# Optimization experiments

Hardware: AMD Instinct MI355X
Metric: run time of the kernel (lower is better)

Reference implementation:

```python
import jax, jax.numpy as jnp
import numpy as np

D_IN = 1024
D_OUT = 1024
NUM_HEADS = 16
HEAD_DIM = D_OUT // NUM_HEADS
SEQ = 2048
BATCH = 2


def setup_inputs() -> dict:
    key = jax.random.key(0)
    ks = jax.random.split(key, 6)
    s = 1.0 / np.sqrt(D_IN)
    x = jax.random.normal(ks[0], (BATCH, SEQ, D_IN), dtype=jnp.float32)
    Wq = jax.random.uniform(ks[1], (D_IN, D_OUT), jnp.float32, -s, s)
    Wk = jax.random.uniform(ks[2], (D_IN, D_OUT), jnp.float32, -s, s)
    Wv = jax.random.uniform(ks[3], (D_IN, D_OUT), jnp.float32, -s, s)
    Wo = jax.random.uniform(ks[4], (D_OUT, D_OUT), jnp.float32, -s, s)
    bo = jax.random.uniform(ks[5], (D_OUT,), jnp.float32, -s, s)
    return {"x": x, "Wq": Wq, "Wk": Wk, "Wv": Wv, "Wo": Wo, "bo": bo}


def reference(x, Wq, Wk, Wv, Wo, bo):
    b, n, _ = x.shape
    # projections, split into heads: (b, h, n, hd)
    def split_heads(t):
        return t.reshape(b, n, NUM_HEADS, HEAD_DIM).transpose(0, 2, 1, 3)
    q = split_heads(x @ Wq)
    k = split_heads(x @ Wk)
    v = split_heads(x @ Wv)
    scores = jnp.einsum("bhqd,bhkd->bhqk", q, k)
    causal = jnp.triu(jnp.ones((n, n), dtype=bool), k=1)
    scores = jnp.where(causal, -jnp.inf, scores)
    attn = jax.nn.softmax(scores / np.sqrt(HEAD_DIM), axis=-1)
    # dropout prob is 0.0 -> identity
    ctx = jnp.einsum("bhqk,bhkd->bhqd", attn, v)
    ctx = ctx.transpose(0, 2, 1, 3).reshape(b, n, D_OUT)
    return ctx @ Wo + bo
```

## Files before the change

kernel.cpp:

```cpp
#include <hip/hip_runtime.h>
#include <hip/hip_bf16.h>
#include <stdint.h>

#define D_IN   1024
#define D_OUT  1024
#define NHEAD  16
#define HDIM   64
#define SEQ    2048
#define BATCH  2
#define M_TOT  (BATCH*SEQ)

typedef __attribute__((ext_vector_type(8)))  short bfx8;
typedef __attribute__((ext_vector_type(4)))  short bfx4;
typedef __attribute__((ext_vector_type(4)))  float fx4;
typedef __attribute__((ext_vector_type(16))) float fx16;
typedef unsigned short u16;
typedef unsigned int   u32;

__device__ __forceinline__ u16 f2bf(float f) {
    u32 u = __builtin_bit_cast(u32, f);
    u32 r = (u + 0x7FFFu + ((u >> 16) & 1u)) >> 16;
    return (u16)r;
}

__device__ __forceinline__ u32 cvtpk(float lo, float hi) {
    u32 r;
    asm("v_cvt_pk_bf16_f32 %0, %1, %2" : "=v"(r) : "v"(lo), "v"(hi));
    return r;
}

__device__ __forceinline__ void gload16(const u16* g, u16* l) {
    __builtin_amdgcn_global_load_lds(
        (const __attribute__((address_space(1))) void*)g,
        (__attribute__((address_space(3))) void*)l, 16, 0, 0);
}

__global__ void k_conv_x(const float* __restrict__ x, u16* __restrict__ xb) {
    int i = blockIdx.x * 256 + threadIdx.x;
    const float4* s = reinterpret_cast<const float4*>(x);
    float4 a = s[2*i], b = s[2*i+1];
    uint4 o;
    o.x = (u32)f2bf(a.x) | ((u32)f2bf(a.y) << 16);
    o.y = (u32)f2bf(a.z) | ((u32)f2bf(a.w) << 16);
    o.z = (u32)f2bf(b.x) | ((u32)f2bf(b.y) << 16);
    o.w = (u32)f2bf(b.z) | ((u32)f2bf(b.w) << 16);
    reinterpret_cast<uint4*>(xb)[i] = o;
}

__global__ void k_conv_wt(const float* __restrict__ Wq, const float* __restrict__ Wk,
                          const float* __restrict__ Wv, const float* __restrict__ Wo,
                          u16* __restrict__ wt) {
    __shared__ float tile[32][33];
    int wsel = blockIdx.z;
    const float* W = (wsel == 0) ? Wq : (wsel == 1) ? Wk : (wsel == 2) ? Wv : Wo;
    const float scale = (wsel == 0) ? 0.125f : 1.0f;
    u16* dst = wt + (size_t)wsel * D_IN * D_OUT;
    int r0 = blockIdx.y * 32, c0 = blockIdx.x * 32;
    int tx = threadIdx.x & 31, ty = threadIdx.x >> 5;
    #pragma unroll
    for (int k = 0; k < 4; k++) {
        int i = ty + k * 8;
        tile[i][tx] = W[(size_t)(r0 + i) * D_OUT + c0 + tx];
    }
    __syncthreads();
    #pragma unroll
    for (int k = 0; k < 4; k++) {
        int i = ty + k * 8;
        dst[(size_t)(c0 + i) * D_IN + r0 + tx] = f2bf(tile[tx][i] * scale);
    }
}

template<int MODE>
__global__ __launch_bounds__(256) void k_gemm128(const u16* __restrict__ A,
                                                 const u16* __restrict__ Bt,
                                                 const float* __restrict__ bias,
                                                 u16* __restrict__ outb,
                                                 float* __restrict__ outf) {
    __shared__ u16 aL[128][32];
    __shared__ u16 bL[128][32];
    const int K = 1024;
    const int nb = blockIdx.x * 128, mb = blockIdx.y * 128;
    const int t = threadIdx.x, lane = t & 63, w = t >> 6;
    const int wr = w >> 1, wc = w & 1;
    const int li = lane & 15, lg = lane >> 4;
    const int srow = lane >> 2, schunk = (lane & 3) * 8;

    fx4 acc[4][4];
    #pragma unroll
    for (int i = 0; i < 4; i++)
        #pragma unroll
        for (int j = 0; j < 4; j++) acc[i][j] = fx4{0.f, 0.f, 0.f, 0.f};

    const u16* aBase = A  + (size_t)(mb + w * 32 + srow) * K + schunk;
    const u16* bBase = Bt + (size_t)(nb + w * 32 + srow) * K + schunk;

    for (int kb = 0; kb < K; kb += 32) {
        #pragma unroll
        for (int c = 0; c < 2; c++) {
            gload16(aBase + (size_t)c * 16 * K + kb, &aL[w * 32 + c * 16][0]);
            gload16(bBase + (size_t)c * 16 * K + kb, &bL[w * 32 + c * 16][0]);
        }
        __syncthreads();
        bfx8 af[4], bf[4];
        #pragma unroll
        for (int mi = 0; mi < 4; mi++)
            af[mi] = *reinterpret_cast<const bfx8*>(&aL[wr * 64 + mi * 16 + li][lg * 8]);
        #pragma unroll
        for (int ni = 0; ni < 4; ni++)
            bf[ni] = *reinterpret_cast<const bfx8*>(&bL[wc * 64 + ni * 16 + li][lg * 8]);
        #pragma unroll
        for (int mi = 0; mi < 4; mi++)
            #pragma unroll
            for (int ni = 0; ni < 4; ni++)
                acc[mi][ni] = __builtin_amdgcn_mfma_f32_16x16x32_bf16(af[mi], bf[ni], acc[mi][ni], 0, 0, 0);
        __syncthreads();
    }

    #pragma unroll
    for (int mi = 0; mi < 4; mi++) {
        #pragma unroll
        for (int ni = 0; ni < 4; ni++) {
            const int n = nb + wc * 64 + ni * 16 + li;
            const int m0 = mb + wr * 64 + mi * 16 + lg * 4;
            if (MODE == 0) {
                const int proj = n >> 10, h = (n >> 6) & 15, d = n & 63;
                const int b = m0 >> 11, s0 = m0 & 2047;
                if (proj == 2) {
                    u16* op = outb + (size_t)2 * M_TOT * D_OUT +
                              ((size_t)(b * NHEAD + h) * HDIM + d) * SEQ + s0;
                    bfx4 pk = {(short)f2bf(acc[mi][ni][0]), (short)f2bf(acc[mi][ni][1]),
                               (short)f2bf(acc[mi][ni][2]), (short)f2bf(acc[mi][ni][3])};
                    *reinterpret_cast<bfx4*>(op) = pk;
                } else {
                    u16* op = outb + (size_t)proj * M_TOT * D_OUT;
                    #pragma unroll
                    for (int r = 0; r < 4; r++)
                        op[((size_t)(b * NHEAD + h) * SEQ + s0 + r) * HDIM + d] =
                            f2bf(acc[mi][ni][r]);
                }
            } else {
                const float bv = bias[n];
                #pragma unroll
                for (int r = 0; r < 4; r++)
                    outf[(size_t)(m0 + r) * D_OUT + n] = acc[mi][ni][r] + bv;
            }
        }
    }
}

__global__ __launch_bounds__(128, 2) void k_attn(const u16* __restrict__ Q,
                                                 const u16* __restrict__ Kp,
                                                 const u16* __restrict__ Vt,
                                                 u16* __restrict__ ctx) {
    __shared__ u16 kbuf[2][64][64];
    __shared__ u16 vbuf[2][64][64];

    const int g    = blockIdx.x;
    const int pid  = g & 255, half = g >> 8;
    const int bh   = pid & 31, jb = pid >> 5;
    const int qi   = (half == 0) ? jb : (half == 1) ? (31 - jb)
                   : (half == 2) ? (8 + jb) : (23 - jb);
    const int ntk  = qi + 1;

    const size_t base = (size_t)bh * SEQ * HDIM;
    const int t = threadIdx.x, lane = t & 63, w = t >> 6;
    const int l31 = lane & 31, hi = lane >> 5;
    const int srow = lane >> 3;
    const int ts = (lane & 7) ^ srow;
    const int bq = bh >> 4, hh = bh & 15;
    const int swz = (l31 & 7) * 8;
    const int qwb = qi * 64 + w * 32;
    const int qg  = qwb + l31;

    auto stage = [&](int bi, int kvb) {
        #pragma unroll
        for (int i = 0; i < 4; i++) {
            const int rb = w * 32 + i * 8;
            const int rr = rb + srow;
            gload16(Kp + base + (size_t)(kvb + rr) * HDIM + ts * 8, &kbuf[bi][rb][0]);
            gload16(Vt + base + (size_t)rr * SEQ + kvb + ts * 8,    &vbuf[bi][rb][0]);
        }
    };

    bfx8 qf[4];
    #pragma unroll
    for (int dc = 0; dc < 4; dc++)
        qf[dc] = *reinterpret_cast<const bfx8*>(
            &Q[base + (size_t)qg * HDIM + dc * 16 + hi * 8]);
    fx16 cacc[2];
    #pragma unroll
    for (int dt = 0; dt < 2; dt++)
        #pragma unroll
        for (int r = 0; r < 16; r++) cacc[dt][r] = 0.f;
    float lsum = 0.f;

    stage(0, 0);
    __syncthreads();

    for (int ti = 0; ti < ntk; ti++) {
        if (ti + 1 < ntk) stage((ti + 1) & 1, (ti + 1) * 64);
        const int bi = ti & 1, kvb = ti * 64;
        fx16 sc[2];
        #pragma unroll
        for (int s = 0; s < 2; s++) {
            #pragma unroll
            for (int r = 0; r < 16; r++) sc[s][r] = 0.f;
            #pragma unroll
            for (int dc = 0; dc < 4; dc++) {
                bfx8 kf = *reinterpret_cast<const bfx8*>(
                    &kbuf[bi][s * 32 + l31][(dc * 16 + hi * 8) ^ swz]);
                sc[s] = __builtin_amdgcn_mfma_f32_32x32x16_bf16(kf, qf[dc], sc[s], 0, 0, 0);
            }
        }
        if (kvb + 63 > qwb) {
            #pragma unroll
            for (int s = 0; s < 2; s++)
                #pragma unroll
                for (int r = 0; r < 16; r++) {
                    int kvg = kvb + s * 32 + (r & 3) + 8 * (r >> 2) + 4 * hi;
                    if (kvg > qg) sc[s][r] = -1e30f;
                }
        }
        float ps = 0.f;
        #pragma unroll
        for (int s = 0; s < 2; s++)
            #pragma unroll
            for (int r = 0; r < 16; r++) {
                float pv = __expf(sc[s][r]);
                sc[s][r] = pv;
                ps += pv;
            }
        lsum += ps;
        #pragma unroll
        for (int c = 0; c < 4; c++) {
            const int s = c >> 1, rb = (c & 1) * 8;
            u32 a0 = cvtpk(sc[s][rb + 0], sc[s][rb + 1]);
            u32 a1 = cvtpk(sc[s][rb + 2], sc[s][rb + 3]);
            u32 b0 = cvtpk(sc[s][rb + 4], sc[s][rb + 5]);
            u32 b1 = cvtpk(sc[s][rb + 6], sc[s][rb + 7]);
            u32 X0 = hi ? a0 : b0, X1 = hi ? a1 : b1;
            u32 Y0 = (u32)__shfl_xor((int)X0, 32);
            u32 Y1 = (u32)__shfl_xor((int)X1, 32);
            uint4 pw;
            pw.x = hi ? Y0 : a0;
            pw.y = hi ? Y1 : a1;
            pw.z = hi ? b0 : Y0;
            pw.w = hi ? b1 : Y1;
            bfx8 pf = __builtin_bit_cast(bfx8, pw);
            #pragma unroll
            for (int dt = 0; dt < 2; dt++) {
                bfx8 vf = *reinterpret_cast<const bfx8*>(
                    &vbuf[bi][dt * 32 + l31][(c * 16 + hi * 8) ^ swz]);
                cacc[dt] = __builtin_amdgcn_mfma_f32_32x32x16_bf16(pf, vf, cacc[dt], 0, 0, 0);
            }
        }
        __syncthreads();
    }

    float ltot = lsum + __shfl_xor(lsum, 32);
    float linv = 1.0f / ltot;
    #pragma unroll
    for (int r = 0; r < 16; r++) {
        const int qpat = (r & 3) + 8 * (r >> 2) + 4 * hi;
        float rl = __shfl(linv, qpat);
        const int q = qwb + qpat;
        #pragma unroll
        for (int dt = 0; dt < 2; dt++)
            ctx[((size_t)(bq * SEQ + q)) * D_OUT + hh * HDIM + dt * 32 + l31] =
                f2bf(cacc[dt][r] * rl);
    }
}

extern "C" void kernel_launch(void* const* d_in, const int* in_sizes, int n_in,
                              void* d_out, int out_size, void* d_ws, size_t ws_size,
                              hipStream_t stream) {
    const float* x  = (const float*)d_in[0];
    const float* Wq = (const float*)d_in[1];
    const float* Wk = (const float*)d_in[2];
    const float* Wv = (const float*)d_in[3];
    const float* Wo = (const float*)d_in[4];
    const float* bo = (const float*)d_in[5];
    float* out = (float*)d_out;

    char* ws = (char*)d_ws;
    u16* xb   = (u16*)(ws);
    u16* wt   = (u16*)(ws + (8u << 20));
    u16* qkvb = (u16*)(ws + (16u << 20));
    u16* ctxb = (u16*)(ws + (40u << 20));

    const u16* Qb  = qkvb;
    const u16* Kb  = qkvb + (size_t)M_TOT * D_OUT;
    const u16* Vtb = qkvb + (size_t)2 * M_TOT * D_OUT;

    k_conv_x <<<2048, 256, 0, stream>>>(x, xb);
    k_conv_wt<<<dim3(32, 32, 4), 256, 0, stream>>>(Wq, Wk, Wv, Wo, wt);
    k_gemm128<0><<<dim3(24, 32), 256, 0, stream>>>(xb, wt, nullptr, qkvb, nullptr);
    k_attn   <<<dim3(1024), 128, 0, stream>>>(Qb, Kb, Vtb, ctxb);
    k_gemm128<1><<<dim3(8, 32), 256, 0, stream>>>(
        ctxb, wt + (size_t)3 * D_IN * D_OUT, bo, nullptr, out);
}
```

Before: 116.1 us.

## Use single-wave attention blocks with explicit vmcnt waits instead of barriers

The attention kernel now runs one 64-thread wavefront per block, each owning a 32-row query tile. The 2048 blocks are scheduled longest-first (descending query tile) with a remapped head order. Because one wave loads and consumes its own LDS K/V tiles, the __syncthreads barriers are replaced by explicit s_waitcnt vmcnt counts on the async global-to-LDS loads. This removes barrier cost and improves load balance, but two blocks with neighbouring query tiles now each load the same K/V, so global traffic per query row roughly doubles. Correctness also depends on the hard-coded vmcnt value matching the number of loads issued per stage.

```diff
diff --git a/kernel.cpp b/kernel.cpp
--- a/kernel.cpp
+++ b/kernel.cpp
@@ -148,37 +148,34 @@
     }
 }
 
-__global__ __launch_bounds__(128, 2) void k_attn(const u16* __restrict__ Q,
-                                                 const u16* __restrict__ Kp,
-                                                 const u16* __restrict__ Vt,
-                                                 u16* __restrict__ ctx) {
+__global__ __launch_bounds__(64) void k_attn(const u16* __restrict__ Q,
+                                             const u16* __restrict__ Kp,
+                                             const u16* __restrict__ Vt,
+                                             u16* __restrict__ ctx) {
     __shared__ u16 kbuf[2][64][64];
     __shared__ u16 vbuf[2][64][64];
 
-    const int g    = blockIdx.x;
-    const int pid  = g & 255, half = g >> 8;
-    const int bh   = pid & 31, jb = pid >> 5;
-    const int qi   = (half == 0) ? jb : (half == 1) ? (31 - jb)
-                   : (half == 2) ? (8 + jb) : (23 - jb);
-    const int ntk  = qi + 1;
+    const int g  = blockIdx.x;
+    const int qi = 63 - (g >> 5);
+    const int m  = g & 31;
+    const int bh = (m & 7) * 4 + (m >> 3);
+    const int ntk = qi / 2 + 1;
 
     const size_t base = (size_t)bh * SEQ * HDIM;
-    const int t = threadIdx.x, lane = t & 63, w = t >> 6;
-    const int l31 = lane & 31, hi = lane >> 5;
+    const int lane = threadIdx.x, l31 = lane & 31, hi = lane >> 5;
     const int srow = lane >> 3;
     const int ts = (lane & 7) ^ srow;
+    const int swz = (l31 & 7) * 8;
+    const int qwb = qi * 32, qg = qwb + l31;
     const int bq = bh >> 4, hh = bh & 15;
-    const int swz = (l31 & 7) * 8;
-    const int qwb = qi * 64 + w * 32;
-    const int qg  = qwb + l31;
 
     auto stage = [&](int bi, int kvb) {
         #pragma unroll
-        for (int i = 0; i < 4; i++) {
-            const int rb = w * 32 + i * 8;
-            const int rr = rb + srow;
-            gload16(Kp + base + (size_t)(kvb + rr) * HDIM + ts * 8, &kbuf[bi][rb][0]);
-            gload16(Vt + base + (size_t)rr * SEQ + kvb + ts * 8,    &vbuf[bi][rb][0]);
+        for (int i = 0; i < 8; i++) {
+            gload16(Kp + base + (size_t)(kvb + i * 8 + srow) * HDIM + ts * 8,
+                    &kbuf[bi][i * 8][0]);
+            gload16(Vt + base + (size_t)(i * 8 + srow) * SEQ + kvb + ts * 8,
+                    &vbuf[bi][i * 8][0]);
         }
     };
 
@@ -195,10 +192,14 @@
     float lsum = 0.f;
 
     stage(0, 0);
-    __syncthreads();
 
     for (int ti = 0; ti < ntk; ti++) {
-        if (ti + 1 < ntk) stage((ti + 1) & 1, (ti + 1) * 64);
+        if (ti + 1 < ntk) {
+            stage((ti + 1) & 1, (ti + 1) * 64);
+            asm volatile("s_waitcnt vmcnt(16)" ::: "memory");
+        } else {
+            asm volatile("s_waitcnt vmcnt(0)" ::: "memory");
+        }
         const int bi = ti & 1, kvb = ti * 64;
         fx16 sc[2];
         #pragma unroll
@@ -254,7 +255,6 @@
                 cacc[dt] = __builtin_amdgcn_mfma_f32_32x32x16_bf16(pf, vf, cacc[dt], 0, 0, 0);
             }
         }
-        __syncthreads();
     }
 
     float ltot = lsum + __shfl_xor(lsum, 32);
@@ -295,7 +295,7 @@
     k_conv_x <<<2048, 256, 0, stream>>>(x, xb);
     k_conv_wt<<<dim3(32, 32, 4), 256, 0, stream>>>(Wq, Wk, Wv, Wo, wt);
     k_gemm128<0><<<dim3(24, 32), 256, 0, stream>>>(xb, wt, nullptr, qkvb, nullptr);
-    k_attn   <<<dim3(1024), 128, 0, stream>>>(Qb, Kb, Vtb, ctxb);
+    k_attn   <<<dim3(2048), 64, 0, stream>>>(Qb, Kb, Vtb, ctxb);
     k_gemm128<1><<<dim3(8, 32), 256, 0, stream>>>(
         ctxb, wt + (size_t)3 * D_IN * D_OUT, bo, nullptr, out);
 }
```

Result: slower. 127.3 us (+9.6%).

## Split attention KV tiles across waves with 32-row query blocks

Applied to the files above, without the earlier changes.

Each attention block now handles 32 query rows instead of 64. Its two waves split every 64-key tile, each wave taking 32 keys, and the partial context accumulators and row sums are combined through shared memory at the end. The grid doubles to 2048 blocks, ordered longest-first (descending query index), with a remapped head index. This gives more parallelism and better load balance on the causal triangle. The cost is re-streaming K/V tiles twice as often per query, plus an extra cross-wave reduction.

```diff
diff --git a/kernel.cpp b/kernel.cpp
--- a/kernel.cpp
+++ b/kernel.cpp
@@ -155,22 +155,20 @@
     __shared__ u16 kbuf[2][64][64];
     __shared__ u16 vbuf[2][64][64];
 
-    const int g    = blockIdx.x;
-    const int pid  = g & 255, half = g >> 8;
-    const int bh   = pid & 31, jb = pid >> 5;
-    const int qi   = (half == 0) ? jb : (half == 1) ? (31 - jb)
-                   : (half == 2) ? (8 + jb) : (23 - jb);
-    const int ntk  = qi + 1;
+    const int g  = blockIdx.x;
+    const int qi = 63 - (g >> 5);
+    const int m  = g & 31;
+    const int bh = (m & 7) * 4 + (m >> 3);
+    const int ntk = qi / 2 + 1;
 
     const size_t base = (size_t)bh * SEQ * HDIM;
     const int t = threadIdx.x, lane = t & 63, w = t >> 6;
     const int l31 = lane & 31, hi = lane >> 5;
     const int srow = lane >> 3;
     const int ts = (lane & 7) ^ srow;
+    const int swz = (l31 & 7) * 8;
+    const int qwb = qi * 32, qg = qwb + l31;
     const int bq = bh >> 4, hh = bh & 15;
-    const int swz = (l31 & 7) * 8;
-    const int qwb = qi * 64 + w * 32;
-    const int qg  = qwb + l31;
 
     auto stage = [&](int bi, int kvb) {
         #pragma unroll
@@ -200,44 +198,37 @@
     for (int ti = 0; ti < ntk; ti++) {
         if (ti + 1 < ntk) stage((ti + 1) & 1, (ti + 1) * 64);
         const int bi = ti & 1, kvb = ti * 64;
-        fx16 sc[2];
-        #pragma unroll
-        for (int s = 0; s < 2; s++) {
-            #pragma unroll
-            for (int r = 0; r < 16; r++) sc[s][r] = 0.f;
-            #pragma unroll
-            for (int dc = 0; dc < 4; dc++) {
-                bfx8 kf = *reinterpret_cast<const bfx8*>(
-                    &kbuf[bi][s * 32 + l31][(dc * 16 + hi * 8) ^ swz]);
-                sc[s] = __builtin_amdgcn_mfma_f32_32x32x16_bf16(kf, qf[dc], sc[s], 0, 0, 0);
-            }
+        fx16 sc;
+        #pragma unroll
+        for (int r = 0; r < 16; r++) sc[r] = 0.f;
+        #pragma unroll
+        for (int dc = 0; dc < 4; dc++) {
+            bfx8 kf = *reinterpret_cast<const bfx8*>(
+                &kbuf[bi][w * 32 + l31][(dc * 16 + hi * 8) ^ swz]);
+            sc = __builtin_amdgcn_mfma_f32_32x32x16_bf16(kf, qf[dc], sc, 0, 0, 0);
         }
         if (kvb + 63 > qwb) {
             #pragma unroll
-            for (int s = 0; s < 2; s++)
-                #pragma unroll
-                for (int r = 0; r < 16; r++) {
-                    int kvg = kvb + s * 32 + (r & 3) + 8 * (r >> 2) + 4 * hi;
-                    if (kvg > qg) sc[s][r] = -1e30f;
-                }
+            for (int r = 0; r < 16; r++) {
+                int kvg = kvb + w * 32 + (r & 3) + 8 * (r >> 2) + 4 * hi;
+                if (kvg > qg) sc[r] = -1e30f;
+            }
         }
         float ps = 0.f;
         #pragma unroll
-        for (int s = 0; s < 2; s++)
-            #pragma unroll
-            for (int r = 0; r < 16; r++) {
-                float pv = __expf(sc[s][r]);
-                sc[s][r] = pv;
-                ps += pv;
-            }
+        for (int r = 0; r < 16; r++) {
+            float pv = __expf(sc[r]);
+            sc[r] = pv;
+            ps += pv;
+        }
         lsum += ps;
         #pragma unroll
-        for (int c = 0; c < 4; c++) {
-            const int s = c >> 1, rb = (c & 1) * 8;
-            u32 a0 = cvtpk(sc[s][rb + 0], sc[s][rb + 1]);
-            u32 a1 = cvtpk(sc[s][rb + 2], sc[s][rb + 3]);
-            u32 b0 = cvtpk(sc[s][rb + 4], sc[s][rb + 5]);
-            u32 b1 = cvtpk(sc[s][rb + 6], sc[s][rb + 7]);
+        for (int cc = 0; cc < 2; cc++) {
+            const int rb = cc * 8;
+            u32 a0 = cvtpk(sc[rb + 0], sc[rb + 1]);
+            u32 a1 = cvtpk(sc[rb + 2], sc[rb + 3]);
+            u32 b0 = cvtpk(sc[rb + 4], sc[rb + 5]);
+            u32 b1 = cvtpk(sc[rb + 6], sc[rb + 7]);
             u32 X0 = hi ? a0 : b0, X1 = hi ? a1 : b1;
             u32 Y0 = (u32)__shfl_xor((int)X0, 32);
             u32 Y1 = (u32)__shfl_xor((int)X1, 32);
@@ -247,27 +238,37 @@
             pw.z = hi ? b0 : Y0;
             pw.w = hi ? b1 : Y1;
             bfx8 pf = __builtin_bit_cast(bfx8, pw);
+            const int ccol = (w * 2 + cc) * 16 + hi * 8;
             #pragma unroll
             for (int dt = 0; dt < 2; dt++) {
                 bfx8 vf = *reinterpret_cast<const bfx8*>(
-                    &vbuf[bi][dt * 32 + l31][(c * 16 + hi * 8) ^ swz]);
+                    &vbuf[bi][dt * 32 + l31][ccol ^ swz]);
                 cacc[dt] = __builtin_amdgcn_mfma_f32_32x32x16_bf16(pf, vf, cacc[dt], 0, 0, 0);
             }
         }
         __syncthreads();
     }
 
-    float ltot = lsum + __shfl_xor(lsum, 32);
-    float linv = 1.0f / ltot;
+    float lt = lsum + __shfl_xor(lsum, 32);
+    float* sb = (float*)&kbuf[0][0][0];
+    float* ls = (float*)&vbuf[0][0][0];
+    const int ow = 1 - w;
     #pragma unroll
     for (int r = 0; r < 16; r++) {
-        const int qpat = (r & 3) + 8 * (r >> 2) + 4 * hi;
-        float rl = __shfl(linv, qpat);
-        const int q = qwb + qpat;
-        #pragma unroll
-        for (int dt = 0; dt < 2; dt++)
-            ctx[((size_t)(bq * SEQ + q)) * D_OUT + hh * HDIM + dt * 32 + l31] =
-                f2bf(cacc[dt][r] * rl);
+        const int qp = (r & 3) + 8 * (r >> 2) + 4 * hi;
+        sb[(ow * 32 + qp) * 32 + l31] = cacc[ow][r];
+    }
+    if (lane < 32) ls[w * 32 + lane] = lt;
+    __syncthreads();
+    float linv = 1.0f / (ls[l31] + ls[32 + l31]);
+    #pragma unroll
+    for (int r = 0; r < 16; r++) {
+        const int qp = (r & 3) + 8 * (r >> 2) + 4 * hi;
+        float rl = __shfl(linv, qp);
+        const int q = qwb + qp;
+        float val = cacc[w][r] + sb[(w * 32 + qp) * 32 + l31];
+        ctx[((size_t)(bq * SEQ + q)) * D_OUT + hh * HDIM + w * 32 + l31] =
+            f2bf(val * rl);
     }
 }
 
@@ -295,7 +296,7 @@
     k_conv_x <<<2048, 256, 0, stream>>>(x, xb);
     k_conv_wt<<<dim3(32, 32, 4), 256, 0, stream>>>(Wq, Wk, Wv, Wo, wt);
     k_gemm128<0><<<dim3(24, 32), 256, 0, stream>>>(xb, wt, nullptr, qkvb, nullptr);
-    k_attn   <<<dim3(1024), 128, 0, stream>>>(Qb, Kb, Vtb, ctxb);
+    k_attn   <<<dim3(2048), 128, 0, stream>>>(Qb, Kb, Vtb, ctxb);
     k_gemm128<1><<<dim3(8, 32), 256, 0, stream>>>(
         ctxb, wt + (size_t)3 * D_IN * D_OUT, bo, nullptr, out);
 }
```

New measurement: 129.7 us. 1.12x slower.

## Double-buffer LDS tiles in GEMM kernel to overlap global loads with MFMA

Applied to the files above, without the earlier changes.

The projection GEMM kernel now uses two LDS buffers for the A and B tiles and issues the direct-to-LDS global loads for the next K-slice before computing on the current one. Explicit vmcnt waits and raw s_barrier replace the two __syncthreads per iteration, so the next tile's loads can stay in flight during the MFMAs. This doubles the LDS footprint per block and depends on the hand-written vmcnt counts matching the number of outstanding loads.

```diff
diff --git a/kernel.cpp b/kernel.cpp
--- a/kernel.cpp
+++ b/kernel.cpp
@@ -76,9 +76,9 @@
                                                  const float* __restrict__ bias,
                                                  u16* __restrict__ outb,
                                                  float* __restrict__ outf) {
-    __shared__ u16 aL[128][32];
-    __shared__ u16 bL[128][32];
-    const int K = 1024;
+    __shared__ u16 aL[2][128][32];
+    __shared__ u16 bL[2][128][32];
+    const int K = 1024, NK = K / 32;
     const int nb = blockIdx.x * 128, mb = blockIdx.y * 128;
     const int t = threadIdx.x, lane = t & 63, w = t >> 6;
     const int wr = w >> 1, wc = w & 1;
@@ -94,26 +94,39 @@
     const u16* aBase = A  + (size_t)(mb + w * 32 + srow) * K + schunk;
     const u16* bBase = Bt + (size_t)(nb + w * 32 + srow) * K + schunk;
 
-    for (int kb = 0; kb < K; kb += 32) {
+    auto stage = [&](int p, int kb) {
         #pragma unroll
         for (int c = 0; c < 2; c++) {
-            gload16(aBase + (size_t)c * 16 * K + kb, &aL[w * 32 + c * 16][0]);
-            gload16(bBase + (size_t)c * 16 * K + kb, &bL[w * 32 + c * 16][0]);
-        }
-        __syncthreads();
+            gload16(aBase + (size_t)c * 16 * K + kb, &aL[p][w * 32 + c * 16][0]);
+            gload16(bBase + (size_t)c * 16 * K + kb, &bL[p][w * 32 + c * 16][0]);
+        }
+    };
+
+    stage(0, 0);
+
+    for (int ti = 0; ti < NK; ti++) {
+        const int p = ti & 1;
+        if (ti + 1 < NK) {
+            stage(p ^ 1, (ti + 1) * 32);
+            asm volatile("s_waitcnt vmcnt(4)" ::: "memory");
+        } else {
+            asm volatile("s_waitcnt vmcnt(0)" ::: "memory");
+        }
+        __builtin_amdgcn_s_barrier();
         bfx8 af[4], bf[4];
         #pragma unroll
         for (int mi = 0; mi < 4; mi++)
-            af[mi] = *reinterpret_cast<const bfx8*>(&aL[wr * 64 + mi * 16 + li][lg * 8]);
+            af[mi] = *reinterpret_cast<const bfx8*>(&aL[p][wr * 64 + mi * 16 + li][lg * 8]);
         #pragma unroll
         for (int ni = 0; ni < 4; ni++)
-            bf[ni] = *reinterpret_cast<const bfx8*>(&bL[wc * 64 + ni * 16 + li][lg * 8]);
+            bf[ni] = *reinterpret_cast<const bfx8*>(&bL[p][wc * 64 + ni * 16 + li][lg * 8]);
         #pragma unroll
         for (int mi = 0; mi < 4; mi++)
             #pragma unroll
             for (int ni = 0; ni < 4; ni++)
                 acc[mi][ni] = __builtin_amdgcn_mfma_f32_16x16x32_bf16(af[mi], bf[ni], acc[mi][ni], 0, 0, 0);
-        __syncthreads();
+        asm volatile("s_waitcnt lgkmcnt(0)" ::: "memory");
+        __builtin_amdgcn_s_barrier();
     }
 
     #pragma unroll
```

Result: slower. 127.6 us (+9.9%).
